# Kernel optimization log

Measured on AMD Instinct MI355X. Metric: run time of the kernel, lower is better.

The kernel has to match this reference:

```python
import jax, jax.numpy as jnp
import numpy as np

EMBED_DIM = 768
NUM_HEADS = 12
SEGMENT_LENGTHS = (2048, 4096, 8192)
DILATION_RATES = (1, 2, 4)
LN_EPS = 1e-5


def setup_inputs() -> dict:
    key = jax.random.key(0)
    ks = jax.random.split(key, 12)
    B, N, E = 2, 8192, EMBED_DIM
    xavier = (2.0 / (E + E)) ** 0.5  # xavier_normal_ std for square weight
    return {
        "query": jax.random.normal(ks[0], (B, N, E), jnp.float32),
        "key_": jax.random.normal(ks[1], (B, N, E), jnp.float32),
        "value": jax.random.normal(ks[2], (B, N, E), jnp.float32),
        "Wq": jax.random.normal(ks[3], (E, E), jnp.float32) * xavier,
        "bq": jnp.zeros((E,), jnp.float32),
        "Wk": jax.random.normal(ks[4], (E, E), jnp.float32) * xavier,
        "bk": jnp.zeros((E,), jnp.float32),
        "Wv": jax.random.normal(ks[5], (E, E), jnp.float32) * xavier,
        "bv": jnp.zeros((E,), jnp.float32),
        "Wo": jax.random.normal(ks[6], (E, E), jnp.float32) * xavier,
        "bo": jnp.zeros((E,), jnp.float32),
        "ln_g": jnp.ones((E,), jnp.float32),
        "ln_b": jnp.zeros((E,), jnp.float32),
    }


def _dilated_attention(q, k, v):
    # q,k,v: [b, n, h, d]  (LongNet dilated attention, non-causal)
    b, n, h, d = q.shape
    G = len(SEGMENT_LENGTHS)
    hpg = h // G  # heads per dilation group
    scale = 1.0 / jnp.sqrt(jnp.asarray(d, q.dtype))
    out = jnp.zeros_like(q)
    for i, (g, r) in enumerate(zip(SEGMENT_LENGTHS, DILATION_RATES)):
        offset = i % r
        hmin, hmax = i * hpg, (i + 1) * hpg
        def seg(x):
            # [b, n_seg, g, h, d] -> dilate within segment, slice head group
            xs = x.reshape(b, n // g, g, h, d)
            return xs[:, :, offset::r, hmin:hmax, :]  # [b, ns, s, hg, d]
        qs, ks_, vs = seg(q), seg(k), seg(v)
        # attention within each dilated segment
        scores = jnp.einsum("bnshd,bnthd->bnhst", qs, ks_) * scale
        attn = jax.nn.softmax(scores, axis=-1)
        xo = jnp.einsum("bnhst,bnthd->bnshd", attn, vs)
        out_r = out.reshape(b, n // g, g, h, d)
        out_r = out_r.at[:, :, offset::r, hmin:hmax, :].add(xo)
        out = out_r.reshape(b, n, h, d)
    return out / G


def reference(query, key_, value, Wq, bq, Wk, bk, Wv, bv, Wo, bo, ln_g, ln_b):
    b, n, e = query.shape
    h, d = NUM_HEADS, e // NUM_HEADS
    q = (query @ Wq.T + bq).reshape(b, n, h, d)
    k = (key_ @ Wk.T + bk).reshape(b, n, h, d)
    v = (value @ Wv.T + bv).reshape(b, n, h, d)
    x = _dilated_attention(q, k, v).reshape(b, n, e)
    mu = jnp.mean(x, axis=-1, keepdims=True)
    var = jnp.mean(jnp.square(x - mu), axis=-1, keepdims=True)
    x = (x - mu) * jax.lax.rsqrt(var + LN_EPS) * ln_g + ln_b
    return x @ Wo.T + bo
```

## Files before the change

kernel.cpp:

```cpp
#include <hip/hip_runtime.h>
#include <hip/hip_bf16.h>
#include <stdint.h>

typedef unsigned int uint32;
typedef unsigned short u16;
typedef __attribute__((ext_vector_type(4))) float f32x4;
typedef __attribute__((ext_vector_type(16))) float f32x16;
typedef __attribute__((ext_vector_type(8))) __bf16 bf16x8;
typedef __attribute__((ext_vector_type(8))) short i16x8;
typedef __attribute__((ext_vector_type(4))) short i16x4;
typedef __attribute__((ext_vector_type(4))) uint32 u32x4;

#define DEVINL static __device__ __forceinline__

DEVINL u16 f2bf(float f){
  uint32 u = __builtin_bit_cast(uint32, f);
  return (u16)((u + 0x7fffu + ((u >> 16) & 1u)) >> 16);
}

DEVINL uint32 cvtpk(float lo, float hi){
  uint32 r;
  asm("v_cvt_pk_bf16_f32 %0, %1, %2" : "=v"(r) : "v"(lo), "v"(hi));
  return r;
}

DEVINL void permswap(uint32 &a, uint32 &b){
  asm volatile("s_nop 1\n\tv_permlane32_swap_b32 %0, %1" : "+v"(a), "+v"(b));
}

DEVINL f32x4 mfma16(bf16x8 a, bf16x8 b, f32x4 c){
  return __builtin_amdgcn_mfma_f32_16x16x32_bf16(a, b, c, 0, 0, 0);
}
DEVINL f32x16 mfma32(bf16x8 a, bf16x8 b, f32x16 c){
  return __builtin_amdgcn_mfma_f32_32x32x16_bf16(a, b, c, 0, 0, 0);
}
DEVINL f32x16 zero16(){
  f32x16 z;
  #pragma unroll
  for (int r = 0; r < 16; ++r) z[r] = 0.f;
  return z;
}

DEVINL void gload16(const u16* g, u16* l){
  __builtin_amdgcn_global_load_lds(
      (const __attribute__((address_space(1))) uint32*)g,
      (__attribute__((address_space(3))) uint32*)l, 16, 0, 0);
}

static constexpr int LDK = 40;
static constexpr size_t ISTR = 2048 * 64;
static constexpr float QSCALE = 0.18033688011112042f;

__global__ void cvt_w(const float* __restrict__ src, u16* __restrict__ dst, int n4){
  int i = blockIdx.x * 256 + threadIdx.x;
  if (i < n4){
    f32x4 v = *(const f32x4*)(src + (size_t)i * 4);
    u16 o[4];
    #pragma unroll
    for (int j = 0; j < 4; ++j) o[j] = f2bf(v[j]);
    *(i16x4*)(dst + (size_t)i * 4) = *(const i16x4*)o;
  }
}

__global__ __launch_bounds__(256) void qkv_gemm(
    const float* __restrict__ X, const u16* __restrict__ W,
    const float* __restrict__ bias, u16* __restrict__ Yg,
    float scale, int tmode)
{
  __shared__ u16 As[128 * LDK];
  __shared__ u16 Bs[128 * LDK];
  const int tid = threadIdx.x;
  const int l = tid & 63, w = tid >> 6;
  const int l15 = l & 15, lh = l >> 4;
  const int wr = w >> 1, wc = w & 1;
  const int row0 = blockIdx.x * 128, col0 = blockIdx.y * 128;
  const int sr = tid >> 1, skc = (tid & 1) * 16;

  const float* ap = X + (size_t)(row0 + sr) * 768 + skc;
  const u16*   bp = W + (size_t)(col0 + sr) * 768 + skc;

  f32x4 acc[4][4];
  #pragma unroll
  for (int i = 0; i < 4; ++i)
    #pragma unroll
    for (int j = 0; j < 4; ++j) acc[i][j] = f32x4{0.f, 0.f, 0.f, 0.f};

  f32x4 ra0, ra1, ra2, ra3; i16x8 rb0, rb1;
  ra0 = *(const f32x4*)(ap);      ra1 = *(const f32x4*)(ap + 4);
  ra2 = *(const f32x4*)(ap + 8);  ra3 = *(const f32x4*)(ap + 12);
  rb0 = *(const i16x8*)(bp);      rb1 = *(const i16x8*)(bp + 8);

  for (int ks = 0; ks < 24; ++ks) {
    __syncthreads();
    u32x4 w0 = { cvtpk(ra0[0], ra0[1]), cvtpk(ra0[2], ra0[3]),
                 cvtpk(ra1[0], ra1[1]), cvtpk(ra1[2], ra1[3]) };
    u32x4 w1 = { cvtpk(ra2[0], ra2[1]), cvtpk(ra2[2], ra2[3]),
                 cvtpk(ra3[0], ra3[1]), cvtpk(ra3[2], ra3[3]) };
    *(i16x8*)&As[sr * LDK + skc]     = __builtin_bit_cast(i16x8, w0);
    *(i16x8*)&As[sr * LDK + skc + 8] = __builtin_bit_cast(i16x8, w1);
    *(i16x8*)&Bs[sr * LDK + skc]     = rb0;
    *(i16x8*)&Bs[sr * LDK + skc + 8] = rb1;
    __syncthreads();
    if (ks < 23) {
      const float* ap2 = ap + (ks + 1) * 32;
      const u16*   bp2 = bp + (ks + 1) * 32;
      ra0 = *(const f32x4*)(ap2);      ra1 = *(const f32x4*)(ap2 + 4);
      ra2 = *(const f32x4*)(ap2 + 8);  ra3 = *(const f32x4*)(ap2 + 12);
      rb0 = *(const i16x8*)(bp2);      rb1 = *(const i16x8*)(bp2 + 8);
    }
    bf16x8 af[4], bfr[4];
    #pragma unroll
    for (int mi = 0; mi < 4; ++mi)
      af[mi] = *(const bf16x8*)&As[(wr * 64 + mi * 16 + l15) * LDK + lh * 8];
    #pragma unroll
    for (int ni = 0; ni < 4; ++ni)
      bfr[ni] = *(const bf16x8*)&Bs[(wc * 64 + ni * 16 + l15) * LDK + lh * 8];
    #pragma unroll
    for (int mi = 0; mi < 4; ++mi)
      #pragma unroll
      for (int ni = 0; ni < 4; ++ni)
        acc[mi][ni] = mfma16(af[mi], bfr[ni], acc[mi][ni]);
  }

  #pragma unroll
  for (int ni = 0; ni < 4; ++ni) {
    const int e = col0 + wc * 64 + ni * 16 + l15;
    const int h = e >> 6, d = e & 63;
    const int grp = h >> 2, hg = h & 3;
    const int instB = (grp == 0) ? 0 : (grp == 1) ? 32 : 48;
    const float bia = bias[e];
    #pragma unroll
    for (int mi = 0; mi < 4; ++mi) {
      #pragma unroll
      for (int r = 0; r < 4; ++r) {
        const int row = row0 + wr * 64 + mi * 16 + lh * 4 + r;
        const int b = row >> 13, nn = row & 8191;
        const int p = nn & ((2048 << grp) - 1);
        if ((p & ((1 << grp) - 1)) != grp) continue;
        const int seg = nn >> (11 + grp);
        const int t = (p - grp) >> grp;
        const int inst = instB + ((b * (4 >> grp) + seg) << 2) + hg;
        const u16 val = f2bf((acc[mi][ni][r] + bia) * scale);
        if (tmode == 0) Yg[(size_t)inst * ISTR + (size_t)t * 64 + d] = val;
        else            Yg[(size_t)inst * ISTR + (size_t)d * 2048 + t] = val;
      }
    }
  }
}

__global__ __launch_bounds__(256) void dil_attn(
    const u16* __restrict__ Qg, const u16* __restrict__ Kg,
    const u16* __restrict__ VgT, uint32* __restrict__ Op32, float* __restrict__ Ls)
{
  __shared__ u16 Kb[2][64 * 64];
  __shared__ u16 Vb[2][64 * 64];
  const int tid = threadIdx.x;
  const int w = tid >> 6, l = tid & 63;
  const int l31 = l & 31, hi = l >> 5;
  const int id = blockIdx.x;
  const int nid = (id & 7) * 112 + (id >> 3);
  const int inst = nid >> 4, qb = nid & 15;
  const size_t ibase = (size_t)inst * ISTR;
  const int qbase = qb * 128 + w * 32;

  const u16* qlane = Qg + ibase + (size_t)(qbase + l31) * 64 + hi * 8;
  const bf16x8 qf0 = *(const bf16x8*)(qlane);
  const bf16x8 qf1 = *(const bf16x8*)(qlane + 16);
  const bf16x8 qf2 = *(const bf16x8*)(qlane + 32);
  const bf16x8 qf3 = *(const bf16x8*)(qlane + 48);

  const int srow = l >> 3;
  const int scol = ((l & 7) ^ (srow & 7)) << 3;
  const u16* kgs = Kg  + ibase + (size_t)srow * 64 + scol;
  const u16* vgs = VgT + ibase + (size_t)srow * 2048 + scol;

  f32x16 acc0 = zero16(), acc1 = zero16();
  float hs = 0.f;
  const int sxor = (l31 & 7) << 3;

  auto STAGE = [&](int buf, int k0){
    #pragma unroll
    for (int q = 0; q < 2; ++q){
      const int rb = w * 16 + q * 8;
      gload16(kgs + (size_t)(k0 + rb) * 64, &Kb[buf][rb * 64]);
      gload16(vgs + (size_t)rb * 2048 + k0, &Vb[buf][rb * 64]);
    }
  };

  STAGE(0, 0);
  asm volatile("s_waitcnt vmcnt(0)");
  __syncthreads();

  int cur = 0;
  for (int step = 0; step < 32; ++step) {
    if (step < 31) STAGE(cur ^ 1, (step + 1) << 6);
    const u16* kt = &Kb[cur][0];
    const u16* vt = &Vb[cur][0];
    #pragma unroll
    for (int s = 0; s < 2; ++s) {
      const int ksub = s * 32;
      const int krow = (ksub + l31) * 64;
      bf16x8 kc0 = *(const bf16x8*)&kt[krow + ((hi * 8)      ^ sxor)];
      bf16x8 kc1 = *(const bf16x8*)&kt[krow + ((16 + hi * 8) ^ sxor)];
      bf16x8 kc2 = *(const bf16x8*)&kt[krow + ((32 + hi * 8) ^ sxor)];
      bf16x8 kc3 = *(const bf16x8*)&kt[krow + ((48 + hi * 8) ^ sxor)];

      f32x16 sT = zero16();
      sT = mfma32(kc0, qf0, sT);
      sT = mfma32(kc1, qf1, sT);
      sT = mfma32(kc2, qf2, sT);
      sT = mfma32(kc3, qf3, sT);

      #pragma unroll
      for (int r = 0; r < 16; ++r) sT[r] = exp2f(sT[r]);
      float s0 = (sT[0] + sT[1]) + (sT[2] + sT[3]);
      float s1 = (sT[4] + sT[5]) + (sT[6] + sT[7]);
      float s2 = (sT[8] + sT[9]) + (sT[10] + sT[11]);
      float s3 = (sT[12] + sT[13]) + (sT[14] + sT[15]);
      hs += (s0 + s1) + (s2 + s3);

      uint32 cw0 = cvtpk(sT[0],  sT[1]),  cw1 = cvtpk(sT[2],  sT[3]);
      uint32 cw2 = cvtpk(sT[4],  sT[5]),  cw3 = cvtpk(sT[6],  sT[7]);
      uint32 cw4 = cvtpk(sT[8],  sT[9]),  cw5 = cvtpk(sT[10], sT[11]);
      uint32 cw6 = cvtpk(sT[12], sT[13]), cw7 = cvtpk(sT[14], sT[15]);
      permswap(cw0, cw2); permswap(cw1, cw3);
      permswap(cw4, cw6); permswap(cw5, cw7);
      bf16x8 pa0 = __builtin_bit_cast(bf16x8, u32x4{cw0, cw1, cw2, cw3});
      bf16x8 pa1 = __builtin_bit_cast(bf16x8, u32x4{cw4, cw5, cw6, cw7});

      const int vr0 = l31 * 64, vr1 = (l31 + 32) * 64;
      bf16x8 v00 = *(const bf16x8*)&vt[vr0 + ((ksub + hi * 8)      ^ sxor)];
      bf16x8 v01 = *(const bf16x8*)&vt[vr0 + ((ksub + 16 + hi * 8) ^ sxor)];
      bf16x8 v10 = *(const bf16x8*)&vt[vr1 + ((ksub + hi * 8)      ^ sxor)];
      bf16x8 v11 = *(const bf16x8*)&vt[vr1 + ((ksub + 16 + hi * 8) ^ sxor)];

      acc0 = mfma32(pa0, v00, acc0);
      acc0 = mfma32(pa1, v01, acc0);
      acc1 = mfma32(pa0, v10, acc1);
      acc1 = mfma32(pa1, v11, acc1);
    }
    asm volatile("s_waitcnt vmcnt(0)");
    __syncthreads();
    cur ^= 1;
  }

  hs += __shfl_xor(hs, 32);
  if (hi == 0) Ls[(size_t)inst * 2048 + qbase + l31] = 1.0f / (3.0f * hs);

  uint32* op = Op32 + ((size_t)inst * 2048 + qbase) * 32 + l31;
  #pragma unroll
  for (int r = 0; r < 16; ++r) {
    const int qrow = (r & 3) + 8 * (r >> 2) + 4 * hi;
    op[(size_t)qrow * 32] = cvtpk(acc0[r], acc1[r]);
  }
}

__global__ __launch_bounds__(256) void ln_gather(
    const uint32* __restrict__ Op32, const float* __restrict__ Ls,
    const float* __restrict__ gamma, const float* __restrict__ beta,
    u16* __restrict__ xln)
{
  const int row = blockIdx.x;
  const int b = row >> 13, nn = row & 8191;
  const int tid = threadIdx.x;
  float v[3];
  #pragma unroll
  for (int j = 0; j < 3; ++j) {
    const int e = tid + j * 256;
    const int h = e >> 6, d = e & 63;
    const int grp = h >> 2, hg = h & 3;
    const int p = nn & ((2048 << grp) - 1);
    float val = 0.f;
    if ((p & ((1 << grp) - 1)) == grp) {
      const int seg = nn >> (11 + grp);
      const int instB = (grp == 0) ? 0 : (grp == 1) ? 32 : 48;
      const int inst = instB + ((b * (4 >> grp) + seg) << 2) + hg;
      const int t = (p - grp) >> grp;
      const uint32 w0 = Op32[((size_t)inst * 2048 + t) * 32 + (d & 31)];
      const float o = __builtin_bit_cast(float, d < 32 ? (w0 << 16) : (w0 & 0xFFFF0000u));
      val = o * Ls[(size_t)inst * 2048 + t];
    }
    v[j] = val;
  }
  float s = v[0] + v[1] + v[2];
  float q = v[0]*v[0] + v[1]*v[1] + v[2]*v[2];
  #pragma unroll
  for (int off = 1; off < 64; off <<= 1) { s += __shfl_xor(s, off); q += __shfl_xor(q, off); }
  __shared__ float red[8];
  const int w = tid >> 6, l = tid & 63;
  if (l == 0) { red[w] = s; red[4 + w] = q; }
  __syncthreads();
  s = red[0] + red[1] + red[2] + red[3];
  q = red[4] + red[5] + red[6] + red[7];
  const float mu = s * (1.f / 768.f);
  const float var = q * (1.f / 768.f) - mu * mu;
  const float rs = rsqrtf(var + 1e-5f);
  #pragma unroll
  for (int j = 0; j < 3; ++j) {
    const int e = tid + j * 256;
    xln[(size_t)row * 768 + e] = f2bf((v[j] - mu) * rs * gamma[e] + beta[e]);
  }
}

__global__ __launch_bounds__(256) void out_gemm(
    const u16* __restrict__ Xb, const u16* __restrict__ W,
    const float* __restrict__ bias, float* __restrict__ out)
{
  __shared__ u16 As[128 * LDK];
  __shared__ u16 Bs[128 * LDK];
  const int tid = threadIdx.x;
  const int l = tid & 63, w = tid >> 6;
  const int l15 = l & 15, lh = l >> 4;
  const int wr = w >> 1, wc = w & 1;
  const int row0 = blockIdx.x * 128, col0 = blockIdx.y * 128;
  const int sr = tid >> 1, skc = (tid & 1) * 16;

  const u16* ap = Xb + (size_t)(row0 + sr) * 768 + skc;
  const u16* bp = W + (size_t)(col0 + sr) * 768 + skc;

  f32x4 acc[4][4];
  #pragma unroll
  for (int i = 0; i < 4; ++i)
    #pragma unroll
    for (int j = 0; j < 4; ++j) acc[i][j] = f32x4{0.f, 0.f, 0.f, 0.f};

  i16x8 ra0, ra1, rb0, rb1;
  ra0 = *(const i16x8*)(ap); ra1 = *(const i16x8*)(ap + 8);
  rb0 = *(const i16x8*)(bp); rb1 = *(const i16x8*)(bp + 8);

  for (int ks = 0; ks < 24; ++ks) {
    __syncthreads();
    *(i16x8*)&As[sr * LDK + skc]     = ra0;
    *(i16x8*)&As[sr * LDK + skc + 8] = ra1;
    *(i16x8*)&Bs[sr * LDK + skc]     = rb0;
    *(i16x8*)&Bs[sr * LDK + skc + 8] = rb1;
    __syncthreads();
    if (ks < 23) {
      const u16* ap2 = ap + (ks + 1) * 32;
      const u16* bp2 = bp + (ks + 1) * 32;
      ra0 = *(const i16x8*)(ap2); ra1 = *(const i16x8*)(ap2 + 8);
      rb0 = *(const i16x8*)(bp2); rb1 = *(const i16x8*)(bp2 + 8);
    }
    bf16x8 af[4], bfr[4];
    #pragma unroll
    for (int mi = 0; mi < 4; ++mi)
      af[mi] = *(const bf16x8*)&As[(wr * 64 + mi * 16 + l15) * LDK + lh * 8];
    #pragma unroll
    for (int ni = 0; ni < 4; ++ni)
      bfr[ni] = *(const bf16x8*)&Bs[(wc * 64 + ni * 16 + l15) * LDK + lh * 8];
    #pragma unroll
    for (int mi = 0; mi < 4; ++mi)
      #pragma unroll
      for (int ni = 0; ni < 4; ++ni)
        acc[mi][ni] = mfma16(af[mi], bfr[ni], acc[mi][ni]);
  }

  #pragma unroll
  for (int ni = 0; ni < 4; ++ni) {
    const int e = col0 + wc * 64 + ni * 16 + l15;
    const float bia = bias[e];
    #pragma unroll
    for (int mi = 0; mi < 4; ++mi) {
      #pragma unroll
      for (int r = 0; r < 4; ++r) {
        const int row = row0 + wr * 64 + mi * 16 + lh * 4 + r;
        out[(size_t)row * 768 + e] = acc[mi][ni][r] + bia;
      }
    }
  }
}

extern "C" void kernel_launch(void* const* d_in, const int* in_sizes, int n_in,
                              void* d_out, int out_size, void* d_ws, size_t ws_size,
                              hipStream_t stream) {
  const float* query = (const float*)d_in[0];
  const float* key_  = (const float*)d_in[1];
  const float* value = (const float*)d_in[2];
  const float* Wq = (const float*)d_in[3];
  const float* bq = (const float*)d_in[4];
  const float* Wk = (const float*)d_in[5];
  const float* bk = (const float*)d_in[6];
  const float* Wv = (const float*)d_in[7];
  const float* bv = (const float*)d_in[8];
  const float* Wo = (const float*)d_in[9];
  const float* bo = (const float*)d_in[10];
  const float* lng = (const float*)d_in[11];
  const float* lnb = (const float*)d_in[12];

  char* ws = (char*)d_ws;
  size_t off = 0;
  auto alloc = [&](size_t bytes) { size_t o = off; off += (bytes + 255) & ~(size_t)255; return o; };
  const size_t WB = 768 * 768 * 2;
  const size_t GB = (size_t)56 * ISTR * 2;
  u16* wqb = (u16*)(ws + alloc(WB));
  u16* wkb = (u16*)(ws + alloc(WB));
  u16* wvb = (u16*)(ws + alloc(WB));
  u16* wob = (u16*)(ws + alloc(WB));
  u16* Qg  = (u16*)(ws + alloc(GB));
  u16* Kg  = (u16*)(ws + alloc(GB));
  u16* VgT = (u16*)(ws + alloc(GB));
  uint32* Op32 = (uint32*)(ws + alloc((size_t)56 * 2048 * 32 * 4));
  float* Lsb  = (float*)(ws + alloc((size_t)56 * 2048 * 4));
  u16* xln = (u16*)(ws + alloc((size_t)16384 * 768 * 2));

  const int n4 = 768 * 768 / 4;
  cvt_w<<<dim3(576), 256, 0, stream>>>(Wq, wqb, n4);
  cvt_w<<<dim3(576), 256, 0, stream>>>(Wk, wkb, n4);
  cvt_w<<<dim3(576), 256, 0, stream>>>(Wv, wvb, n4);
  cvt_w<<<dim3(576), 256, 0, stream>>>(Wo, wob, n4);

  qkv_gemm<<<dim3(128, 6), 256, 0, stream>>>(query, wqb, bq, Qg, QSCALE, 0);
  qkv_gemm<<<dim3(128, 6), 256, 0, stream>>>(key_,  wkb, bk, Kg, 1.0f, 0);
  qkv_gemm<<<dim3(128, 6), 256, 0, stream>>>(value, wvb, bv, VgT, 1.0f, 1);

  dil_attn<<<dim3(896), 256, 0, stream>>>(Qg, Kg, VgT, Op32, Lsb);
  ln_gather<<<dim3(16384), 256, 0, stream>>>(Op32, Lsb, lng, lnb, xln);
  out_gemm<<<dim3(128, 6), 256, 0, stream>>>(xln, wob, bo, (float*)d_out);
}
```

Baseline: 324.1 us.

## Split attention KV range across two blocks and compute row sums via MFMA

```diff
diff --git a/kernel.cpp b/kernel.cpp
--- a/kernel.cpp
+++ b/kernel.cpp
@@ -158,10 +158,12 @@
   const int w = tid >> 6, l = tid & 63;
   const int l31 = l & 31, hi = l >> 5;
   const int id = blockIdx.x;
-  const int nid = (id & 7) * 112 + (id >> 3);
-  const int inst = nid >> 4, qb = nid & 15;
+  const int nid = (id & 7) * 224 + (id >> 3);
+  const int inst = nid >> 5, rem = nid & 31;
+  const int qb = rem >> 1, kh = rem & 1;
   const size_t ibase = (size_t)inst * ISTR;
   const int qbase = qb * 128 + w * 32;
+  const int k0base = kh * 1024;
 
   const u16* qlane = Qg + ibase + (size_t)(qbase + l31) * 64 + hi * 8;
   const bf16x8 qf0 = *(const bf16x8*)(qlane);
@@ -174,9 +176,10 @@
   const u16* kgs = Kg  + ibase + (size_t)srow * 64 + scol;
   const u16* vgs = VgT + ibase + (size_t)srow * 2048 + scol;
 
-  f32x16 acc0 = zero16(), acc1 = zero16();
-  float hs = 0.f;
+  f32x16 acc0 = zero16(), acc1 = zero16(), rs = zero16();
   const int sxor = (l31 & 7) << 3;
+  const bf16x8 ones = __builtin_bit_cast(bf16x8,
+      u32x4{0x3F803F80u, 0x3F803F80u, 0x3F803F80u, 0x3F803F80u});
 
   auto STAGE = [&](int buf, int k0){
     #pragma unroll
@@ -187,13 +190,13 @@
     }
   };
 
-  STAGE(0, 0);
+  STAGE(0, k0base);
   asm volatile("s_waitcnt vmcnt(0)");
   __syncthreads();
 
   int cur = 0;
-  for (int step = 0; step < 32; ++step) {
-    if (step < 31) STAGE(cur ^ 1, (step + 1) << 6);
+  for (int step = 0; step < 16; ++step) {
+    if (step < 15) STAGE(cur ^ 1, k0base + ((step + 1) << 6));
     const u16* kt = &Kb[cur][0];
     const u16* vt = &Vb[cur][0];
     #pragma unroll
@@ -212,12 +215,7 @@
       sT = mfma32(kc3, qf3, sT);
 
       #pragma unroll
-      for (int r = 0; r < 16; ++r) sT[r] = exp2f(sT[r]);
-      float s0 = (sT[0] + sT[1]) + (sT[2] + sT[3]);
-      float s1 = (sT[4] + sT[5]) + (sT[6] + sT[7]);
-      float s2 = (sT[8] + sT[9]) + (sT[10] + sT[11]);
-      float s3 = (sT[12] + sT[13]) + (sT[14] + sT[15]);
-      hs += (s0 + s1) + (s2 + s3);
+      for (int r = 0; r < 16; ++r) sT[r] = __builtin_amdgcn_exp2f(sT[r]);
 
       uint32 cw0 = cvtpk(sT[0],  sT[1]),  cw1 = cvtpk(sT[2],  sT[3]);
       uint32 cw2 = cvtpk(sT[4],  sT[5]),  cw3 = cvtpk(sT[6],  sT[7]);
@@ -234,6 +232,8 @@
       bf16x8 v10 = *(const bf16x8*)&vt[vr1 + ((ksub + hi * 8)      ^ sxor)];
       bf16x8 v11 = *(const bf16x8*)&vt[vr1 + ((ksub + 16 + hi * 8) ^ sxor)];
 
+      rs   = mfma32(pa0, ones, rs);
+      rs   = mfma32(pa1, ones, rs);
       acc0 = mfma32(pa0, v00, acc0);
       acc0 = mfma32(pa1, v01, acc0);
       acc1 = mfma32(pa0, v10, acc1);
@@ -244,10 +244,16 @@
     cur ^= 1;
   }
 
-  hs += __shfl_xor(hs, 32);
-  if (hi == 0) Ls[(size_t)inst * 2048 + qbase + l31] = 1.0f / (3.0f * hs);
-
-  uint32* op = Op32 + ((size_t)inst * 2048 + qbase) * 32 + l31;
+  if (l31 == 0) {
+    float* lsp = Ls + ((size_t)kh * 56 + inst) * 2048 + qbase;
+    #pragma unroll
+    for (int r = 0; r < 16; ++r) {
+      const int qrow = (r & 3) + 8 * (r >> 2) + 4 * hi;
+      lsp[qrow] = rs[r];
+    }
+  }
+  uint32* op = Op32 + (size_t)kh * (56u * 2048u * 32u)
+                    + ((size_t)inst * 2048 + qbase) * 32 + l31;
   #pragma unroll
   for (int r = 0; r < 16; ++r) {
     const int qrow = (r & 3) + 8 * (r >> 2) + 4 * hi;
@@ -263,6 +269,7 @@
   const int row = blockIdx.x;
   const int b = row >> 13, nn = row & 8191;
   const int tid = threadIdx.x;
+  const size_t KHOFF = 56u * 2048u * 32u;
   float v[3];
   #pragma unroll
   for (int j = 0; j < 3; ++j) {
@@ -276,9 +283,13 @@
       const int instB = (grp == 0) ? 0 : (grp == 1) ? 32 : 48;
       const int inst = instB + ((b * (4 >> grp) + seg) << 2) + hg;
       const int t = (p - grp) >> grp;
-      const uint32 w0 = Op32[((size_t)inst * 2048 + t) * 32 + (d & 31)];
-      const float o = __builtin_bit_cast(float, d < 32 ? (w0 << 16) : (w0 & 0xFFFF0000u));
-      val = o * Ls[(size_t)inst * 2048 + t];
+      const size_t wbase = ((size_t)inst * 2048 + t) * 32 + (d & 31);
+      const uint32 w0 = Op32[wbase];
+      const uint32 w1 = Op32[wbase + KHOFF];
+      const float o0 = __builtin_bit_cast(float, d < 32 ? (w0 << 16) : (w0 & 0xFFFF0000u));
+      const float o1 = __builtin_bit_cast(float, d < 32 ? (w1 << 16) : (w1 & 0xFFFF0000u));
+      const float s = Ls[(size_t)inst * 2048 + t] + Ls[(size_t)(56 * 2048) + inst * 2048 + t];
+      val = (o0 + o1) * (1.0f / (3.0f * s));
     }
     v[j] = val;
   }
@@ -399,8 +410,8 @@
   u16* Qg  = (u16*)(ws + alloc(GB));
   u16* Kg  = (u16*)(ws + alloc(GB));
   u16* VgT = (u16*)(ws + alloc(GB));
-  uint32* Op32 = (uint32*)(ws + alloc((size_t)56 * 2048 * 32 * 4));
-  float* Lsb  = (float*)(ws + alloc((size_t)56 * 2048 * 4));
+  uint32* Op32 = (uint32*)(ws + alloc((size_t)2 * 56 * 2048 * 32 * 4));
+  float* Lsb  = (float*)(ws + alloc((size_t)2 * 56 * 2048 * 4));
   u16* xln = (u16*)(ws + alloc((size_t)16384 * 768 * 2));
 
   const int n4 = 768 * 768 / 4;
@@ -413,7 +424,7 @@
   qkv_gemm<<<dim3(128, 6), 256, 0, stream>>>(key_,  wkb, bk, Kg, 1.0f, 0);
   qkv_gemm<<<dim3(128, 6), 256, 0, stream>>>(value, wvb, bv, VgT, 1.0f, 1);
 
-  dil_attn<<<dim3(896), 256, 0, stream>>>(Qg, Kg, VgT, Op32, Lsb);
+  dil_attn<<<dim3(1792), 256, 0, stream>>>(Qg, Kg, VgT, Op32, Lsb);
   ln_gather<<<dim3(16384), 256, 0, stream>>>(Op32, Lsb, lng, lnb, xln);
   out_gemm<<<dim3(128, 6), 256, 0, stream>>>(xln, wob, bo, (float*)d_out);
 }
```

After: 298.4 us. 7.9% less time.
